# Kernel optimization log

Hardware: AMD Instinct MI355X
Metric: run time of the kernel (lower is better)

The kernel has to match this reference:

```python
import jax, jax.numpy as jnp
import numpy as np

N = 300000   # nodes
D = 128      # in_feats == dim (linears4 consumes attention output)
H = 8        # num_heads
K = 5        # fixed mailbox size (reducer_k pads neighbor list to 5)
EPS = 1e-5


def _layer_norm(x, g, b):
    m = jnp.mean(x, axis=-1, keepdims=True)
    v = jnp.mean((x - m) ** 2, axis=-1, keepdims=True)
    return (x - m) * jax.lax.rsqrt(v + EPS) * g + b


def _self_atten(q, k, v, mask, wq, wk, wv, wo, bo, w1, b1, w2, b2, g1, be1, g2, be2):
    # q: [N,1,D], k/v: [N,K,D], mask: [N,1,1,K] (True = padded key)
    n = q.shape[0]
    dh = D // H
    def heads(x):  # [n, s, D] -> [n, H, s, dh]
        return x.reshape(n, -1, H, dh).transpose(0, 2, 1, 3)
    q1, k1, v1 = heads(q @ wq), heads(k @ wk), heads(v @ wv)
    dots = jnp.einsum('nhqd,nhkd->nhqk', q1, k1) * (dh ** -0.5)
    dots = jnp.where(mask, -jnp.inf, dots)
    attn = jax.nn.softmax(dots, axis=-1)
    out = jnp.einsum('nhqk,nhkd->nhqd', attn, v1)
    out = out.transpose(0, 2, 1, 3).reshape(n, -1, D) @ wo + bo
    x = _layer_norm(q + out, g1, be1)            # residual + norm1
    ffn = jax.nn.relu(x @ w1 + b1) @ w2 + b2
    return _layer_norm(x + ffn, g2, be2)         # residual + norm2


def setup_inputs() -> dict:
    key = jax.random.key(0)
    ks = iter(jax.random.split(key, 64))
    nrm = lambda shape, s=0.05: jax.random.normal(next(ks), shape, jnp.float32) * s
    feat = jax.random.normal(next(ks), (N, D), jnp.float32)
    nbr_idx = jax.random.randint(next(ks), (N, K), 0, N, dtype=jnp.int32)
    deg = jax.random.randint(next(ks), (N,), 1, K + 1)      # in-degree in [1, 5]
    nbr_valid = jnp.arange(K)[None, :] < deg[:, None]        # [N, K] bool
    inp = {'feat': feat, 'nbr_idx': nbr_idx, 'nbr_valid': nbr_valid}
    for i in ('1', '2'):
        inp['wq' + i] = nrm((D, D)); inp['wk' + i] = nrm((D, D)); inp['wv' + i] = nrm((D, D))
        inp['wo' + i] = nrm((D, D)); inp['bo' + i] = jnp.zeros((D,), jnp.float32)
        inp['w' + i + 'a'] = nrm((D, 2 * D)); inp['b' + i + 'a'] = jnp.zeros((2 * D,), jnp.float32)
        inp['w' + i + 'b'] = nrm((2 * D, D)); inp['b' + i + 'b'] = jnp.zeros((D,), jnp.float32)
        inp['g' + i + 'a'] = jnp.ones((D,), jnp.float32); inp['be' + i + 'a'] = jnp.zeros((D,), jnp.float32)
        inp['g' + i + 'b'] = jnp.ones((D,), jnp.float32); inp['be' + i + 'b'] = jnp.zeros((D,), jnp.float32)
    inp['w4'] = nrm((D, D // 2)); inp['b4'] = jnp.zeros((D // 2,), jnp.float32)
    return inp


def reference(feat, nbr_idx, nbr_valid,
              wq1, wk1, wv1, wo1, bo1, w1a, b1a, w1b, b1b, g1a, be1a, g1b, be1b,
              wq2, wk2, wv2, wo2, bo2, w2a, b2a, w2b, b2b, g2a, be2a, g2b, be2b,
              w4, b4):
    # mailbox gather: padded [N, K, D] neighbor features, zeros in padding slots
    k = feat[nbr_idx] * nbr_valid[..., None].astype(feat.dtype)
    q = feat[:, None, :]                                   # [N, 1, D]
    mask = (jnp.sum(k, axis=-1) == 0)[:, None, None, :]    # count_pad -> [N,1,1,K]
    q = _self_atten(q, k, k, mask, wq1, wk1, wv1, wo1, bo1, w1a, b1a, w1b, b1b, g1a, be1a, g1b, be1b)
    out = _self_atten(q, k, k, mask, wq2, wk2, wv2, wo2, bo2, w2a, b2a, w2b, b2b, g2a, be2a, g2b, be2b)
    return jnp.tanh(out[:, 0, :] @ w4 + b4)                # tanh(linears4(hf)) -> [N, D//2]
```

## Files before the change

### kernel.cpp

```cpp
#include <hip/hip_runtime.h>
#include <cstdint>
#include <cmath>

using u16 = unsigned short;
using u8  = unsigned char;
using u32 = unsigned int;

typedef __attribute__((ext_vector_type(8))) short short8;
typedef __attribute__((ext_vector_type(8))) unsigned short u16x8;
typedef __attribute__((ext_vector_type(4))) float f32x4;

#define DEV static __device__ __forceinline__

DEV u16 f2bf(float f) {
  u32 u = __builtin_bit_cast(u32, f);
  u = u + 0x7fffu + ((u >> 16) & 1u);
  return (u16)(u >> 16);
}
DEV float bf2f(u16 h) { return __builtin_bit_cast(float, ((u32)h) << 16); }

template<int NT, int NKB>
DEV void gemm_direct(const u16* __restrict__ wsrc, int ncols,
                     const u16* act, int strideA, int kbase,
                     f32x4* acc, int rt, int cbase, int lane) {
  int l15 = lane & 15, quad = lane >> 4;
  const u16* arow = act + (rt*16 + l15) * strideA + kbase + quad*8;
#pragma unroll
  for (int kb = 0; kb < NKB; ++kb) {
    short8 af = *(const short8*)(arow + kb*32);
    const u16* wrow = wsrc + (size_t)(kb*4 + quad) * ncols * 8;
#pragma unroll
    for (int t = 0; t < NT; ++t) {
      short8 bf = *(const short8*)(wrow + ((cbase + t)*16 + l15) * 8);
      acc[t] = __builtin_amdgcn_mfma_f32_16x16x32_bf16(af, bf, acc[t], 0, 0, 0);
    }
  }
}

DEV void ln_epi(f32x4* acc, float rxf[4][4], int rt, int cbase, int wave, int lane,
                const float* __restrict__ bias, const float* __restrict__ g,
                const float* __restrict__ be, u16* act, float* red) {
  int l15 = lane & 15, quad = lane >> 4;
  int half = wave & 1;
  float v[4][4];
  float s[4] = {0.f,0.f,0.f,0.f}, ss[4] = {0.f,0.f,0.f,0.f};
#pragma unroll
  for (int t = 0; t < 4; ++t) {
    int col = (cbase + t)*16 + l15;
    float b = bias[col];
#pragma unroll
    for (int r = 0; r < 4; ++r) {
      float val = acc[t][r] + b + rxf[t][r];
      v[t][r] = val;
      s[r] += val; ss[r] += val*val;
    }
  }
#pragma unroll
  for (int m = 1; m < 16; m <<= 1) {
#pragma unroll
    for (int r = 0; r < 4; ++r) {
      s[r]  += __shfl_xor(s[r],  m);
      ss[r] += __shfl_xor(ss[r], m);
    }
  }
  if (l15 == 0) {
#pragma unroll
    for (int r = 0; r < 4; ++r) {
      int row = rt*16 + quad*4 + r;
      red[row*4 + half*2 + 0] = s[r];
      red[row*4 + half*2 + 1] = ss[r];
    }
  }
  __syncthreads();
#pragma unroll
  for (int r = 0; r < 4; ++r) {
    int row = rt*16 + quad*4 + r;
    float st  = red[row*4 + 0] + red[row*4 + 2];
    float sst = red[row*4 + 1] + red[row*4 + 3];
    float mean = st * (1.f/128.f);
    float var  = sst * (1.f/128.f) - mean*mean;
    float rs = rsqrtf(var + 1e-5f);
#pragma unroll
    for (int t = 0; t < 4; ++t) {
      int col = (cbase + t)*16 + l15;
      float xn = (v[t][r] - mean) * rs * g[col] + be[col];
      rxf[t][r] = xn;
      act[row*136 + col] = f2bf(xn);
    }
  }
  __syncthreads();
}

DEV void relu_epi(f32x4* acc, int rt, int cbase, int lane,
                  const float* __restrict__ bias, int colbase, u16* h1) {
  int l15 = lane & 15, quad = lane >> 4;
#pragma unroll
  for (int t = 0; t < 4; ++t) {
    int col = (cbase + t)*16 + l15;
    float b = bias[colbase + col];
#pragma unroll
    for (int r = 0; r < 4; ++r) {
      int row = rt*16 + quad*4 + r;
      float val = fmaxf(acc[t][r] + b, 0.f);
      h1[row*264 + colbase + col] = f2bf(val);
    }
  }
}

DEV void q_epi(f32x4* acc, int rt, int cbase, int lane, u16* dst) {
  int l15 = lane & 15, quad = lane >> 4;
#pragma unroll
  for (int t = 0; t < 4; ++t)
#pragma unroll
    for (int r = 0; r < 4; ++r)
      dst[(rt*16 + quad*4 + r)*264 + (cbase + t)*16 + l15] = f2bf(acc[t][r]);
}

DEV void attention(const u16* __restrict__ Pg, const int* s_nidx, const u8* s_nval,
                   const u16* qbuf, u16* act, int layerOff, int tid) {
  int nl = tid >> 3, h = tid & 7;
  float q[16];
  {
    const u16* qp = qbuf + nl*264 + h*16;
    u16x8 q0 = *(const u16x8*)qp;
    u16x8 q1 = *(const u16x8*)(qp + 8);
#pragma unroll
    for (int i = 0; i < 8; ++i) { q[i] = bf2f(q0[i]); q[8+i] = bf2f(q1[i]); }
  }
  float sc[5], w[5];
  int mlist[5], vmask[5];
  float mx = -1e30f;
#pragma unroll
  for (int j = 0; j < 5; ++j) {
    int mj = s_nidx[nl*5 + j];
    int vj = s_nval[nl*5 + j];
    mlist[j] = mj; vmask[j] = vj;
    const u16* kr = Pg + (size_t)mj*512 + layerOff + h*16;
    u16x8 k0 = *(const u16x8*)kr;
    u16x8 k1 = *(const u16x8*)(kr + 8);
    float d = 0.f;
#pragma unroll
    for (int i = 0; i < 8; ++i) d += bf2f(k0[i])*q[i] + bf2f(k1[i])*q[8+i];
    sc[j] = vj ? d * 0.25f : -1e30f;
    mx = fmaxf(mx, sc[j]);
  }
  int anyv = vmask[0] | vmask[1] | vmask[2] | vmask[3] | vmask[4];
  float sum = 0.f;
#pragma unroll
  for (int j = 0; j < 5; ++j) { w[j] = vmask[j] ? __expf(sc[j] - mx) : 0.f; sum += w[j]; }
  float o[16];
#pragma unroll
  for (int i = 0; i < 16; ++i) o[i] = 0.f;
  if (anyv) {
    float inv = 1.f / sum;
#pragma unroll
    for (int j = 0; j < 5; ++j) {
      if (w[j] > 0.f) {
        const u16* vr = Pg + (size_t)mlist[j]*512 + layerOff + 128 + h*16;
        u16x8 v0 = *(const u16x8*)vr;
        u16x8 v1 = *(const u16x8*)(vr + 8);
        float wj = w[j] * inv;
#pragma unroll
        for (int i = 0; i < 8; ++i) { o[i] += wj * bf2f(v0[i]); o[8+i] += wj * bf2f(v1[i]); }
      }
    }
  }
  u16* op = act + nl*136 + h*16;
#pragma unroll
  for (int i = 0; i < 16; ++i) op[i] = f2bf(o[i]);
}

__global__ __launch_bounds__(512) void k1_proj(const float* __restrict__ feat,
                                               u16* __restrict__ P,
                                               const u16* __restrict__ wpack, int N) {
  __shared__ __align__(16) u16 s_act[64*136];
  __shared__ __align__(16) u16 s_c[64*128];
  int tid = threadIdx.x;
  int base = blockIdx.x * 64;
  {
    int row = tid >> 3, c0 = (tid & 7) * 16;
    int n = base + row;
    float v[16];
    if (n < N) {
      const float4* fp = (const float4*)(feat + (size_t)n*128 + c0);
#pragma unroll
      for (int q = 0; q < 4; ++q) { float4 f = fp[q]; v[q*4]=f.x; v[q*4+1]=f.y; v[q*4+2]=f.z; v[q*4+3]=f.w; }
    } else {
#pragma unroll
      for (int i = 0; i < 16; ++i) v[i] = 0.f;
    }
#pragma unroll
    for (int i = 0; i < 16; ++i) s_act[row*136 + c0 + i] = f2bf(v[i]);
  }
  __syncthreads();
  int wave = tid >> 6, lane = tid & 63;
  int rt = wave >> 1, cbase = (wave & 1) * 4;
  int l15 = lane & 15, quad = lane >> 4;
  f32x4 z = {0.f,0.f,0.f,0.f};
  for (int wsel = 0; wsel < 4; ++wsel) {
    f32x4 acc[4] = {z,z,z,z};
    gemm_direct<4,4>(wpack + (size_t)(1 + wsel)*16384, 128, s_act, 136, 0, acc, rt, cbase, lane);
    __syncthreads();
#pragma unroll
    for (int t = 0; t < 4; ++t)
#pragma unroll
      for (int r = 0; r < 4; ++r)
        s_c[(rt*16 + quad*4 + r)*128 + (cbase + t)*16 + l15] = f2bf(acc[t][r]);
    __syncthreads();
    const uint4* src = (const uint4*)s_c;
    for (int i = tid; i < 1024; i += 512) {
      int row = i >> 4, c8 = i & 15;
      int n = base + row;
      if (n < N) *(uint4*)(P + (size_t)n*512 + wsel*128 + c8*8) = src[i];
    }
  }
}

struct K2Args {
  const float* feat; const int* nidx; const void* nval; const int* flag;
  const u16* P; const u16* wpack;
  const float* bo1; const float* b1a; const float* b1b;
  const float* g1a; const float* be1a; const float* g1b; const float* be1b;
  const float* bo2; const float* b2a; const float* b2b;
  const float* g2a; const float* be2a; const float* g2b; const float* be2b;
  const float* b4; float* out; int N;
};

__global__ __launch_bounds__(256) void k2_fused(K2Args a) {
  __shared__ __align__(16) u16   s_act[32*136];
  __shared__ __align__(16) u16   s_h1[32*264];
  __shared__ float s_red[32*4];
  __shared__ int   s_nidx[160];
  __shared__ u8    s_nval[160];

  int tid = threadIdx.x;
  int base = blockIdx.x * 32;
  int wave = tid >> 6, lane = tid & 63;
  int rt = wave >> 1, cb4 = (wave & 1) * 4, cb2 = (wave & 1) * 2;
  int l15 = lane & 15, quad = lane >> 4;

  {
    float* sF = (float*)s_h1;
    int row = tid >> 3, c0 = (tid & 7) * 16;
    int n = base + row;
    float v[16];
    if (n < a.N) {
      const float4* fp = (const float4*)(a.feat + (size_t)n*128 + c0);
#pragma unroll
      for (int q = 0; q < 4; ++q) { float4 f = fp[q]; v[q*4]=f.x; v[q*4+1]=f.y; v[q*4+2]=f.z; v[q*4+3]=f.w; }
    } else {
#pragma unroll
      for (int i = 0; i < 16; ++i) v[i] = 0.f;
    }
#pragma unroll
    for (int i = 0; i < 16; ++i) sF[row*132 + c0 + i] = v[i];
  }
  {
    int mode = *a.flag;
    for (int i = tid; i < 160; i += 256) {
      int n2 = base + i/5;
      int idx = 0; u8 val = 0;
      if (n2 < a.N) {
        size_t e = (size_t)base*5 + i;
        idx = a.nidx[e];
        if (mode == 0)      val = (((const int*)a.nval)[e]   != 0);
        else if (mode == 1) val = (((const float*)a.nval)[e] != 0.f);
        else                val = (((const u8*)a.nval)[e]    != 0);
      }
      s_nidx[i] = idx; s_nval[i] = val;
    }
  }
  __syncthreads();

  float rxf[4][4];
  {
    const float* sF = (const float*)s_h1;
#pragma unroll
    for (int t = 0; t < 4; ++t) {
      int col = (cb4 + t)*16 + l15;
#pragma unroll
      for (int r = 0; r < 4; ++r) {
        int row = rt*16 + quad*4 + r;
        float f = sF[row*132 + col];
        rxf[t][r] = f;
        s_act[row*136 + col] = f2bf(f);
      }
    }
  }
  __syncthreads();

  f32x4 z = {0.f,0.f,0.f,0.f};
  const u16* wp = a.wpack;

  {
    f32x4 acc[4] = {z,z,z,z};
    gemm_direct<4,4>(wp + 0, 128, s_act, 136, 0, acc, rt, cb4, lane);
    q_epi(acc, rt, cb4, lane, s_h1);
    __syncthreads();
  }
  attention(a.P, s_nidx, s_nval, s_h1, s_act, 0, tid);
  __syncthreads();
  {
    f32x4 acc[4] = {z,z,z,z};
    gemm_direct<4,4>(wp + (size_t)5*16384, 128, s_act, 136, 0, acc, rt, cb4, lane);
    ln_epi(acc, rxf, rt, cb4, wave, lane, a.bo1, a.g1a, a.be1a, s_act, s_red);
  }
  {
    f32x4 acc[4] = {z,z,z,z};
    gemm_direct<4,4>(wp + (size_t)6*16384, 128, s_act, 136, 0, acc, rt, cb4, lane);
    relu_epi(acc, rt, cb4, lane, a.b1a, 0, s_h1);
    f32x4 acc2[4] = {z,z,z,z};
    gemm_direct<4,4>(wp + (size_t)7*16384, 128, s_act, 136, 0, acc2, rt, cb4, lane);
    relu_epi(acc2, rt, cb4, lane, a.b1a, 128, s_h1);
    __syncthreads();
  }
  {
    f32x4 acc[4] = {z,z,z,z};
    gemm_direct<4,4>(wp + (size_t)8*16384, 128, s_h1, 264, 0,   acc, rt, cb4, lane);
    gemm_direct<4,4>(wp + (size_t)9*16384, 128, s_h1, 264, 128, acc, rt, cb4, lane);
    ln_epi(acc, rxf, rt, cb4, wave, lane, a.b1b, a.g1b, a.be1b, s_act, s_red);
  }
  {
    f32x4 acc[4] = {z,z,z,z};
    gemm_direct<4,4>(wp + (size_t)10*16384, 128, s_act, 136, 0, acc, rt, cb4, lane);
    q_epi(acc, rt, cb4, lane, s_h1);
    __syncthreads();
  }
  attention(a.P, s_nidx, s_nval, s_h1, s_act, 256, tid);
  __syncthreads();
  {
    f32x4 acc[4] = {z,z,z,z};
    gemm_direct<4,4>(wp + (size_t)11*16384, 128, s_act, 136, 0, acc, rt, cb4, lane);
    ln_epi(acc, rxf, rt, cb4, wave, lane, a.bo2, a.g2a, a.be2a, s_act, s_red);
  }
  {
    f32x4 acc[4] = {z,z,z,z};
    gemm_direct<4,4>(wp + (size_t)12*16384, 128, s_act, 136, 0, acc, rt, cb4, lane);
    relu_epi(acc, rt, cb4, lane, a.b2a, 0, s_h1);
    f32x4 acc2[4] = {z,z,z,z};
    gemm_direct<4,4>(wp + (size_t)13*16384, 128, s_act, 136, 0, acc2, rt, cb4, lane);
    relu_epi(acc2, rt, cb4, lane, a.b2a, 128, s_h1);
    __syncthreads();
  }
  {
    f32x4 acc[4] = {z,z,z,z};
    gemm_direct<4,4>(wp + (size_t)14*16384, 128, s_h1, 264, 0,   acc, rt, cb4, lane);
    gemm_direct<4,4>(wp + (size_t)15*16384, 128, s_h1, 264, 128, acc, rt, cb4, lane);
    ln_epi(acc, rxf, rt, cb4, wave, lane, a.b2b, a.g2b, a.be2b, s_act, s_red);
  }
  {
    f32x4 acc[2] = {z,z};
    gemm_direct<2,4>(wp + (size_t)16*16384, 64, s_act, 136, 0, acc, rt, cb2, lane);
#pragma unroll
    for (int t = 0; t < 2; ++t) {
      int col = (cb2 + t)*16 + l15;
      float b = a.b4[col];
#pragma unroll
      for (int r = 0; r < 4; ++r) {
        int row = rt*16 + quad*4 + r;
        int n = base + row;
        if (n < a.N) a.out[(size_t)n*64 + col] = tanhf(acc[t][r] + b);
      }
    }
  }
}

struct PackDesc { const float* src; int srcStride; int row0; int col0; int ncols; int dstOff; };
struct PackArgs { PackDesc d[17]; };

__global__ void pack_kernel(PackArgs pa, u16* __restrict__ wpack) {
  PackDesc d = pa.d[blockIdx.x];
  int total = 128 * d.ncols;
  for (int e = threadIdx.x; e < total; e += blockDim.x) {
    int k, n;
    if (d.ncols == 128) { k = e >> 7; n = e & 127; }
    else                { k = e >> 6; n = e & 63; }
    float v = d.src[(size_t)(d.row0 + k) * d.srcStride + d.col0 + n];
    int kb = k >> 5, q = (k >> 3) & 3, j = k & 7;
    wpack[d.dstOff + ((kb*4 + q) * d.ncols + n) * 8 + j] = f2bf(v);
  }
}

__global__ void detect_kernel(const u32* __restrict__ nv, int* __restrict__ flag) {
  __shared__ int sInt, sFlt;
  if (threadIdx.x == 0) { sInt = 1; sFlt = 1; }
  __syncthreads();
  int okI = 1, okF = 1;
  for (int i = threadIdx.x; i < 2048; i += blockDim.x) {
    u32 w = nv[i];
    if (w > 1u) okI = 0;
    if (w != 0u && w != 0x3F800000u) okF = 0;
  }
  if (!okI) atomicAnd(&sInt, 0);
  if (!okF) atomicAnd(&sFlt, 0);
  __syncthreads();
  if (threadIdx.x == 0) *flag = sInt ? 0 : (sFlt ? 1 : 2);
}

extern "C" void kernel_launch(void* const* d_in, const int* in_sizes, int n_in,
                              void* d_out, int out_size, void* d_ws, size_t ws_size,
                              hipStream_t stream) {
  const float* feat = (const float*)d_in[0];
  const int*   nidx = (const int*)d_in[1];
  const void*  nval = d_in[2];
  int N = in_sizes[0] / 128;

  u16* P     = (u16*)d_ws;
  u16* wpack = P + (size_t)N * 512;
  int* flag  = (int*)(wpack + (size_t)17 * 16384);

  detect_kernel<<<1, 256, 0, stream>>>((const u32*)nval, flag);

  PackArgs pa;
  int c = 0;
  auto W = [&](int i){ return (const float*)d_in[i]; };
  auto add = [&](const float* src, int stride, int r0, int c0, int ncols){
    pa.d[c] = PackDesc{src, stride, r0, c0, ncols, c * 16384}; ++c;
  };
  add(W(3),  128, 0,   0,   128);
  add(W(4),  128, 0,   0,   128);
  add(W(5),  128, 0,   0,   128);
  add(W(17), 128, 0,   0,   128);
  add(W(18), 128, 0,   0,   128);
  add(W(6),  128, 0,   0,   128);
  add(W(8),  256, 0,   0,   128);
  add(W(8),  256, 0,   128, 128);
  add(W(10), 128, 0,   0,   128);
  add(W(10), 128, 128, 0,   128);
  add(W(16), 128, 0,   0,   128);
  add(W(19), 128, 0,   0,   128);
  add(W(21), 256, 0,   0,   128);
  add(W(21), 256, 0,   128, 128);
  add(W(23), 128, 0,   0,   128);
  add(W(23), 128, 128, 0,   128);
  add(W(29), 64,  0,   0,   64);
  pack_kernel<<<17, 256, 0, stream>>>(pa, wpack);

  k1_proj<<<(N + 63) / 64, 512, 0, stream>>>(feat, P, wpack, N);

  K2Args ka;
  ka.feat = feat; ka.nidx = nidx; ka.nval = nval; ka.flag = flag;
  ka.P = P; ka.wpack = wpack;
  ka.bo1 = W(7);  ka.b1a = W(9);  ka.b1b = W(11);
  ka.g1a = W(12); ka.be1a = W(13); ka.g1b = W(14); ka.be1b = W(15);
  ka.bo2 = W(20); ka.b2a = W(22); ka.b2b = W(24);
  ka.g2a = W(25); ka.be2a = W(26); ka.g2b = W(27); ka.be2b = W(28);
  ka.b4 = W(30); ka.out = (float*)d_out; ka.N = N;
  k2_fused<<<(N + 31) / 32, 256, 0, stream>>>(ka);
}
```

Measured before the change: 1.046 ms.

## Make each wave own 16 full rows to remove block-level barriers

Both kernels are restructured so each wave handles 16 nodes across all 128 output columns, with private shared-memory slices. LayerNorm row reductions then stay inside one wave's shuffles, so the shared reduction buffer and every __syncthreads are removed. Each wave also stages its own features, neighbor lists and attention work, and the residual is read straight from global memory. In exchange each wave holds twice as many accumulators (8 tiles instead of 4), which raises register pressure and may reduce occupancy.

```diff
diff --git a/kernel.cpp b/kernel.cpp
--- a/kernel.cpp
+++ b/kernel.cpp
@@ -8,6 +8,7 @@
 
 typedef __attribute__((ext_vector_type(8))) short short8;
 typedef __attribute__((ext_vector_type(8))) unsigned short u16x8;
+typedef __attribute__((ext_vector_type(4))) unsigned short u16x4;
 typedef __attribute__((ext_vector_type(4))) float f32x4;
 
 #define DEV static __device__ __forceinline__
@@ -20,33 +21,31 @@
 DEV float bf2f(u16 h) { return __builtin_bit_cast(float, ((u32)h) << 16); }
 
 template<int NT, int NKB>
-DEV void gemm_direct(const u16* __restrict__ wsrc, int ncols,
-                     const u16* act, int strideA, int kbase,
-                     f32x4* acc, int rt, int cbase, int lane) {
+DEV void gemm_wave(const u16* __restrict__ wsrc, int ncols,
+                   const u16* actp, int strideA, int kbase,
+                   f32x4* acc, int lane) {
   int l15 = lane & 15, quad = lane >> 4;
-  const u16* arow = act + (rt*16 + l15) * strideA + kbase + quad*8;
+  const u16* arow = actp + l15 * strideA + kbase + quad*8;
 #pragma unroll
   for (int kb = 0; kb < NKB; ++kb) {
     short8 af = *(const short8*)(arow + kb*32);
     const u16* wrow = wsrc + (size_t)(kb*4 + quad) * ncols * 8;
 #pragma unroll
     for (int t = 0; t < NT; ++t) {
-      short8 bf = *(const short8*)(wrow + ((cbase + t)*16 + l15) * 8);
+      short8 bf = *(const short8*)(wrow + (t*16 + l15) * 8);
       acc[t] = __builtin_amdgcn_mfma_f32_16x16x32_bf16(af, bf, acc[t], 0, 0, 0);
     }
   }
 }
 
-DEV void ln_epi(f32x4* acc, float rxf[4][4], int rt, int cbase, int wave, int lane,
-                const float* __restrict__ bias, const float* __restrict__ g,
-                const float* __restrict__ be, u16* act, float* red) {
-  int l15 = lane & 15, quad = lane >> 4;
-  int half = wave & 1;
-  float v[4][4];
+DEV void ln_epi8(f32x4* acc, float rxf[8][4], int l15, int quad,
+                 const float* __restrict__ bias, const float* __restrict__ g,
+                 const float* __restrict__ be, u16* actp) {
+  float v[8][4];
   float s[4] = {0.f,0.f,0.f,0.f}, ss[4] = {0.f,0.f,0.f,0.f};
 #pragma unroll
-  for (int t = 0; t < 4; ++t) {
-    int col = (cbase + t)*16 + l15;
+  for (int t = 0; t < 8; ++t) {
+    int col = t*16 + l15;
     float b = bias[col];
 #pragma unroll
     for (int r = 0; r < 4; ++r) {
@@ -63,154 +62,143 @@
       ss[r] += __shfl_xor(ss[r], m);
     }
   }
-  if (l15 == 0) {
-#pragma unroll
-    for (int r = 0; r < 4; ++r) {
-      int row = rt*16 + quad*4 + r;
-      red[row*4 + half*2 + 0] = s[r];
-      red[row*4 + half*2 + 1] = ss[r];
-    }
-  }
-  __syncthreads();
 #pragma unroll
   for (int r = 0; r < 4; ++r) {
-    int row = rt*16 + quad*4 + r;
-    float st  = red[row*4 + 0] + red[row*4 + 2];
-    float sst = red[row*4 + 1] + red[row*4 + 3];
-    float mean = st * (1.f/128.f);
-    float var  = sst * (1.f/128.f) - mean*mean;
+    int row = quad*4 + r;
+    float mean = s[r] * (1.f/128.f);
+    float var  = ss[r] * (1.f/128.f) - mean*mean;
     float rs = rsqrtf(var + 1e-5f);
 #pragma unroll
-    for (int t = 0; t < 4; ++t) {
-      int col = (cbase + t)*16 + l15;
+    for (int t = 0; t < 8; ++t) {
+      int col = t*16 + l15;
       float xn = (v[t][r] - mean) * rs * g[col] + be[col];
       rxf[t][r] = xn;
-      act[row*136 + col] = f2bf(xn);
-    }
-  }
-  __syncthreads();
-}
-
-DEV void relu_epi(f32x4* acc, int rt, int cbase, int lane,
-                  const float* __restrict__ bias, int colbase, u16* h1) {
-  int l15 = lane & 15, quad = lane >> 4;
-#pragma unroll
-  for (int t = 0; t < 4; ++t) {
-    int col = (cbase + t)*16 + l15;
+      actp[row*136 + col] = f2bf(xn);
+    }
+  }
+}
+
+DEV void relu_epi8(f32x4* acc, int l15, int quad,
+                   const float* __restrict__ bias, int colbase, u16* hb) {
+#pragma unroll
+  for (int t = 0; t < 8; ++t) {
+    int col = t*16 + l15;
     float b = bias[colbase + col];
 #pragma unroll
     for (int r = 0; r < 4; ++r) {
-      int row = rt*16 + quad*4 + r;
-      float val = fmaxf(acc[t][r] + b, 0.f);
-      h1[row*264 + colbase + col] = f2bf(val);
-    }
-  }
-}
-
-DEV void q_epi(f32x4* acc, int rt, int cbase, int lane, u16* dst) {
-  int l15 = lane & 15, quad = lane >> 4;
-#pragma unroll
-  for (int t = 0; t < 4; ++t)
+      int row = quad*4 + r;
+      hb[row*264 + colbase + col] = f2bf(fmaxf(acc[t][r] + b, 0.f));
+    }
+  }
+}
+
+DEV void q_epi8(f32x4* acc, int l15, int quad, u16* hb) {
+#pragma unroll
+  for (int t = 0; t < 8; ++t)
 #pragma unroll
     for (int r = 0; r < 4; ++r)
-      dst[(rt*16 + quad*4 + r)*264 + (cbase + t)*16 + l15] = f2bf(acc[t][r]);
-}
-
-DEV void attention(const u16* __restrict__ Pg, const int* s_nidx, const u8* s_nval,
-                   const u16* qbuf, u16* act, int layerOff, int tid) {
-  int nl = tid >> 3, h = tid & 7;
-  float q[16];
-  {
-    const u16* qp = qbuf + nl*264 + h*16;
-    u16x8 q0 = *(const u16x8*)qp;
-    u16x8 q1 = *(const u16x8*)(qp + 8);
-#pragma unroll
-    for (int i = 0; i < 8; ++i) { q[i] = bf2f(q0[i]); q[8+i] = bf2f(q1[i]); }
-  }
-  float sc[5], w[5];
-  int mlist[5], vmask[5];
-  float mx = -1e30f;
-#pragma unroll
-  for (int j = 0; j < 5; ++j) {
-    int mj = s_nidx[nl*5 + j];
-    int vj = s_nval[nl*5 + j];
-    mlist[j] = mj; vmask[j] = vj;
-    const u16* kr = Pg + (size_t)mj*512 + layerOff + h*16;
-    u16x8 k0 = *(const u16x8*)kr;
-    u16x8 k1 = *(const u16x8*)(kr + 8);
-    float d = 0.f;
-#pragma unroll
-    for (int i = 0; i < 8; ++i) d += bf2f(k0[i])*q[i] + bf2f(k1[i])*q[8+i];
-    sc[j] = vj ? d * 0.25f : -1e30f;
-    mx = fmaxf(mx, sc[j]);
-  }
-  int anyv = vmask[0] | vmask[1] | vmask[2] | vmask[3] | vmask[4];
-  float sum = 0.f;
-#pragma unroll
-  for (int j = 0; j < 5; ++j) { w[j] = vmask[j] ? __expf(sc[j] - mx) : 0.f; sum += w[j]; }
-  float o[16];
-#pragma unroll
-  for (int i = 0; i < 16; ++i) o[i] = 0.f;
-  if (anyv) {
-    float inv = 1.f / sum;
+      hb[(quad*4 + r)*264 + t*16 + l15] = f2bf(acc[t][r]);
+}
+
+DEV void attention_wave(const u16* __restrict__ Pg, const int* nidx, const u8* nval,
+                        const u16* qb, u16* actp, int layerOff, int lane) {
+#pragma unroll
+  for (int p = 0; p < 2; ++p) {
+    int nl = p*8 + (lane >> 3);
+    int hd = lane & 7;
+    float q[16];
+    {
+      const u16* qp = qb + nl*264 + hd*16;
+      u16x8 q0 = *(const u16x8*)qp;
+      u16x8 q1 = *(const u16x8*)(qp + 8);
+#pragma unroll
+      for (int i = 0; i < 8; ++i) { q[i] = bf2f(q0[i]); q[8+i] = bf2f(q1[i]); }
+    }
+    float sc[5], w[5];
+    int mlist[5], vmask[5];
+    float mx = -1e30f;
 #pragma unroll
     for (int j = 0; j < 5; ++j) {
-      if (w[j] > 0.f) {
-        const u16* vr = Pg + (size_t)mlist[j]*512 + layerOff + 128 + h*16;
-        u16x8 v0 = *(const u16x8*)vr;
-        u16x8 v1 = *(const u16x8*)(vr + 8);
-        float wj = w[j] * inv;
-#pragma unroll
-        for (int i = 0; i < 8; ++i) { o[i] += wj * bf2f(v0[i]); o[8+i] += wj * bf2f(v1[i]); }
+      int mj = nidx[nl*5 + j];
+      int vj = nval[nl*5 + j];
+      mlist[j] = mj; vmask[j] = vj;
+      const u16* kr = Pg + (size_t)mj*512 + layerOff + hd*16;
+      u16x8 k0 = *(const u16x8*)kr;
+      u16x8 k1 = *(const u16x8*)(kr + 8);
+      float d = 0.f;
+#pragma unroll
+      for (int i = 0; i < 8; ++i) d += bf2f(k0[i])*q[i] + bf2f(k1[i])*q[8+i];
+      sc[j] = vj ? d * 0.25f : -1e30f;
+      mx = fmaxf(mx, sc[j]);
+    }
+    int anyv = vmask[0] | vmask[1] | vmask[2] | vmask[3] | vmask[4];
+    float sum = 0.f;
+#pragma unroll
+    for (int j = 0; j < 5; ++j) { w[j] = vmask[j] ? __expf(sc[j] - mx) : 0.f; sum += w[j]; }
+    float o[16];
+#pragma unroll
+    for (int i = 0; i < 16; ++i) o[i] = 0.f;
+    if (anyv) {
+      float inv = 1.f / sum;
+#pragma unroll
+      for (int j = 0; j < 5; ++j) {
+        if (w[j] > 0.f) {
+          const u16* vr = Pg + (size_t)mlist[j]*512 + layerOff + 128 + hd*16;
+          u16x8 v0 = *(const u16x8*)vr;
+          u16x8 v1 = *(const u16x8*)(vr + 8);
+          float wj = w[j] * inv;
+#pragma unroll
+          for (int i = 0; i < 8; ++i) { o[i] += wj * bf2f(v0[i]); o[8+i] += wj * bf2f(v1[i]); }
+        }
       }
     }
-  }
-  u16* op = act + nl*136 + h*16;
-#pragma unroll
-  for (int i = 0; i < 16; ++i) op[i] = f2bf(o[i]);
-}
-
-__global__ __launch_bounds__(512) void k1_proj(const float* __restrict__ feat,
+    u16* op = actp + nl*136 + hd*16;
+#pragma unroll
+    for (int i = 0; i < 16; ++i) op[i] = f2bf(o[i]);
+  }
+}
+
+DEV void stage_feat_wave(const float* __restrict__ feat, int nb, int N, u16* actp, int lane) {
+#pragma unroll
+  for (int it = 0; it < 8; ++it) {
+    int i = it*64 + lane;
+    int row = i >> 5, c4 = i & 31;
+    int n = nb + row;
+    float4 f = {0.f,0.f,0.f,0.f};
+    if (n < N) f = *(const float4*)(feat + (size_t)n*128 + c4*4);
+    u16x4 v4 = { f2bf(f.x), f2bf(f.y), f2bf(f.z), f2bf(f.w) };
+    *(u16x4*)(actp + row*136 + c4*4) = v4;
+  }
+}
+
+__global__ __launch_bounds__(256) void k1_proj(const float* __restrict__ feat,
                                                u16* __restrict__ P,
                                                const u16* __restrict__ wpack, int N) {
-  __shared__ __align__(16) u16 s_act[64*136];
-  __shared__ __align__(16) u16 s_c[64*128];
-  int tid = threadIdx.x;
-  int base = blockIdx.x * 64;
-  {
-    int row = tid >> 3, c0 = (tid & 7) * 16;
-    int n = base + row;
-    float v[16];
-    if (n < N) {
-      const float4* fp = (const float4*)(feat + (size_t)n*128 + c0);
-#pragma unroll
-      for (int q = 0; q < 4; ++q) { float4 f = fp[q]; v[q*4]=f.x; v[q*4+1]=f.y; v[q*4+2]=f.z; v[q*4+3]=f.w; }
-    } else {
-#pragma unroll
-      for (int i = 0; i < 16; ++i) v[i] = 0.f;
-    }
-#pragma unroll
-    for (int i = 0; i < 16; ++i) s_act[row*136 + c0 + i] = f2bf(v[i]);
-  }
-  __syncthreads();
-  int wave = tid >> 6, lane = tid & 63;
-  int rt = wave >> 1, cbase = (wave & 1) * 4;
+  __shared__ __align__(16) u16 s_act[4*16*136];
+  __shared__ __align__(16) u16 s_c[4*16*128];
+  int tid = threadIdx.x, wave = tid >> 6, lane = tid & 63;
   int l15 = lane & 15, quad = lane >> 4;
+  u16* actp = s_act + wave*16*136;
+  u16* cbuf = s_c   + wave*16*128;
+  int nb = blockIdx.x*64 + wave*16;
+
+  stage_feat_wave(feat, nb, N, actp, lane);
+
   f32x4 z = {0.f,0.f,0.f,0.f};
   for (int wsel = 0; wsel < 4; ++wsel) {
-    f32x4 acc[4] = {z,z,z,z};
-    gemm_direct<4,4>(wpack + (size_t)(1 + wsel)*16384, 128, s_act, 136, 0, acc, rt, cbase, lane);
-    __syncthreads();
-#pragma unroll
-    for (int t = 0; t < 4; ++t)
+    f32x4 acc[8] = {z,z,z,z,z,z,z,z};
+    gemm_wave<8,4>(wpack + (size_t)(1 + wsel)*16384, 128, actp, 136, 0, acc, lane);
+#pragma unroll
+    for (int t = 0; t < 8; ++t)
 #pragma unroll
       for (int r = 0; r < 4; ++r)
-        s_c[(rt*16 + quad*4 + r)*128 + (cbase + t)*16 + l15] = f2bf(acc[t][r]);
-    __syncthreads();
-    const uint4* src = (const uint4*)s_c;
-    for (int i = tid; i < 1024; i += 512) {
+        cbuf[(quad*4 + r)*128 + t*16 + l15] = f2bf(acc[t][r]);
+    const uint4* src = (const uint4*)cbuf;
+#pragma unroll
+    for (int it = 0; it < 4; ++it) {
+      int i = it*64 + lane;
       int row = i >> 4, c8 = i & 15;
-      int n = base + row;
+      int n = nb + row;
       if (n < N) *(uint4*)(P + (size_t)n*512 + wsel*128 + c8*8) = src[i];
     }
   }
@@ -227,138 +215,111 @@
 };
 
 __global__ __launch_bounds__(256) void k2_fused(K2Args a) {
-  __shared__ __align__(16) u16   s_act[32*136];
-  __shared__ __align__(16) u16   s_h1[32*264];
-  __shared__ float s_red[32*4];
-  __shared__ int   s_nidx[160];
-  __shared__ u8    s_nval[160];
-
-  int tid = threadIdx.x;
-  int base = blockIdx.x * 32;
-  int wave = tid >> 6, lane = tid & 63;
-  int rt = wave >> 1, cb4 = (wave & 1) * 4, cb2 = (wave & 1) * 2;
+  __shared__ __align__(16) u16 s_act[4*16*136];
+  __shared__ __align__(16) u16 s_h[4*16*264];
+  __shared__ int s_nidx[4*80];
+  __shared__ u8  s_nval[4*80];
+
+  int tid = threadIdx.x, wave = tid >> 6, lane = tid & 63;
   int l15 = lane & 15, quad = lane >> 4;
-
-  {
-    float* sF = (float*)s_h1;
-    int row = tid >> 3, c0 = (tid & 7) * 16;
-    int n = base + row;
-    float v[16];
-    if (n < a.N) {
-      const float4* fp = (const float4*)(a.feat + (size_t)n*128 + c0);
-#pragma unroll
-      for (int q = 0; q < 4; ++q) { float4 f = fp[q]; v[q*4]=f.x; v[q*4+1]=f.y; v[q*4+2]=f.z; v[q*4+3]=f.w; }
-    } else {
-#pragma unroll
-      for (int i = 0; i < 16; ++i) v[i] = 0.f;
-    }
-#pragma unroll
-    for (int i = 0; i < 16; ++i) sF[row*132 + c0 + i] = v[i];
-  }
+  u16* actp = s_act + wave*16*136;
+  u16* hb   = s_h   + wave*16*264;
+  int* wn_i = s_nidx + wave*80;
+  u8*  wn_v = s_nval + wave*80;
+  int nb = blockIdx.x*64 + wave*16;
+
+  stage_feat_wave(a.feat, nb, a.N, actp, lane);
+
   {
     int mode = *a.flag;
-    for (int i = tid; i < 160; i += 256) {
-      int n2 = base + i/5;
+    for (int i = lane; i < 80; i += 64) {
+      int n2 = nb + i/5;
       int idx = 0; u8 val = 0;
       if (n2 < a.N) {
-        size_t e = (size_t)base*5 + i;
+        size_t e = (size_t)nb*5 + i;
         idx = a.nidx[e];
         if (mode == 0)      val = (((const int*)a.nval)[e]   != 0);
         else if (mode == 1) val = (((const float*)a.nval)[e] != 0.f);
         else                val = (((const u8*)a.nval)[e]    != 0);
       }
-      s_nidx[i] = idx; s_nval[i] = val;
-    }
-  }
-  __syncthreads();
-
-  float rxf[4][4];
-  {
-    const float* sF = (const float*)s_h1;
-#pragma unroll
-    for (int t = 0; t < 4; ++t) {
-      int col = (cb4 + t)*16 + l15;
-#pragma unroll
-      for (int r = 0; r < 4; ++r) {
-        int row = rt*16 + quad*4 + r;
-        float f = sF[row*132 + col];
-        rxf[t][r] = f;
-        s_act[row*136 + col] = f2bf(f);
-      }
-    }
-  }
-  __syncthreads();
+      wn_i[i] = idx; wn_v[i] = val;
+    }
+  }
+
+  float rxf[8][4];
+#pragma unroll
+  for (int t = 0; t < 8; ++t) {
+    int col = t*16 + l15;
+#pragma unroll
+    for (int r = 0; r < 4; ++r) {
+      int n = nb + quad*4 + r;
+      rxf[t][r] = (n < a.N) ? a.feat[(size_t)n*128 + col] : 0.f;
+    }
+  }
 
   f32x4 z = {0.f,0.f,0.f,0.f};
   const u16* wp = a.wpack;
 
   {
+    f32x4 acc[8] = {z,z,z,z,z,z,z,z};
+    gemm_wave<8,4>(wp + 0, 128, actp, 136, 0, acc, lane);
+    q_epi8(acc, l15, quad, hb);
+  }
+  attention_wave(a.P, wn_i, wn_v, hb, actp, 0, lane);
+  {
+    f32x4 acc[8] = {z,z,z,z,z,z,z,z};
+    gemm_wave<8,4>(wp + (size_t)5*16384, 128, actp, 136, 0, acc, lane);
+    ln_epi8(acc, rxf, l15, quad, a.bo1, a.g1a, a.be1a, actp);
+  }
+  {
+    f32x4 acc[8] = {z,z,z,z,z,z,z,z};
+    gemm_wave<8,4>(wp + (size_t)6*16384, 128, actp, 136, 0, acc, lane);
+    relu_epi8(acc, l15, quad, a.b1a, 0, hb);
+    f32x4 acc2[8] = {z,z,z,z,z,z,z,z};
+    gemm_wave<8,4>(wp + (size_t)7*16384, 128, actp, 136, 0, acc2, lane);
+    relu_epi8(acc2, l15, quad, a.b1a, 128, hb);
+  }
+  {
+    f32x4 acc[8] = {z,z,z,z,z,z,z,z};
+    gemm_wave<8,4>(wp + (size_t)8*16384, 128, hb, 264, 0,   acc, lane);
+    gemm_wave<8,4>(wp + (size_t)9*16384, 128, hb, 264, 128, acc, lane);
+    ln_epi8(acc, rxf, l15, quad, a.b1b, a.g1b, a.be1b, actp);
+  }
+  {
+    f32x4 acc[8] = {z,z,z,z,z,z,z,z};
+    gemm_wave<8,4>(wp + (size_t)10*16384, 128, actp, 136, 0, acc, lane);
+    q_epi8(acc, l15, quad, hb);
+  }
+  attention_wave(a.P, wn_i, wn_v, hb, actp, 256, lane);
+  {
+    f32x4 acc[8] = {z,z,z,z,z,z,z,z};
+    gemm_wave<8,4>(wp + (size_t)11*16384, 128, actp, 136, 0, acc, lane);
+    ln_epi8(acc, rxf, l15, quad, a.bo2, a.g2a, a.be2a, actp);
+  }
+  {
+    f32x4 acc[8] = {z,z,z,z,z,z,z,z};
+    gemm_wave<8,4>(wp + (size_t)12*16384, 128, actp, 136, 0, acc, lane);
+    relu_epi8(acc, l15, quad, a.b2a, 0, hb);
+    f32x4 acc2[8] = {z,z,z,z,z,z,z,z};
+    gemm_wave<8,4>(wp + (size_t)13*16384, 128, actp, 136, 0, acc2, lane);
+    relu_epi8(acc2, l15, quad, a.b2a, 128, hb);
+  }
+  {
+    f32x4 acc[8] = {z,z,z,z,z,z,z,z};
+    gemm_wave<8,4>(wp + (size_t)14*16384, 128, hb, 264, 0,   acc, lane);
+    gemm_wave<8,4>(wp + (size_t)15*16384, 128, hb, 264, 128, acc, lane);
+    ln_epi8(acc, rxf, l15, quad, a.b2b, a.g2b, a.be2b, actp);
+  }
+  {
     f32x4 acc[4] = {z,z,z,z};
-    gemm_direct<4,4>(wp + 0, 128, s_act, 136, 0, acc, rt, cb4, lane);
-    q_epi(acc, rt, cb4, lane, s_h1);
-    __syncthreads();
-  }
-  attention(a.P, s_nidx, s_nval, s_h1, s_act, 0, tid);
-  __syncthreads();
-  {
-    f32x4 acc[4] = {z,z,z,z};
-    gemm_direct<4,4>(wp + (size_t)5*16384, 128, s_act, 136, 0, acc, rt, cb4, lane);
-    ln_epi(acc, rxf, rt, cb4, wave, lane, a.bo1, a.g1a, a.be1a, s_act, s_red);
-  }
-  {
-    f32x4 acc[4] = {z,z,z,z};
-    gemm_direct<4,4>(wp + (size_t)6*16384, 128, s_act, 136, 0, acc, rt, cb4, lane);
-    relu_epi(acc, rt, cb4, lane, a.b1a, 0, s_h1);
-    f32x4 acc2[4] = {z,z,z,z};
-    gemm_direct<4,4>(wp + (size_t)7*16384, 128, s_act, 136, 0, acc2, rt, cb4, lane);
-    relu_epi(acc2, rt, cb4, lane, a.b1a, 128, s_h1);
-    __syncthreads();
-  }
-  {
-    f32x4 acc[4] = {z,z,z,z};
-    gemm_direct<4,4>(wp + (size_t)8*16384, 128, s_h1, 264, 0,   acc, rt, cb4, lane);
-    gemm_direct<4,4>(wp + (size_t)9*16384, 128, s_h1, 264, 128, acc, rt, cb4, lane);
-    ln_epi(acc, rxf, rt, cb4, wave, lane, a.b1b, a.g1b, a.be1b, s_act, s_red);
-  }
-  {
-    f32x4 acc[4] = {z,z,z,z};
-    gemm_direct<4,4>(wp + (size_t)10*16384, 128, s_act, 136, 0, acc, rt, cb4, lane);
-    q_epi(acc, rt, cb4, lane, s_h1);
-    __syncthreads();
-  }
-  attention(a.P, s_nidx, s_nval, s_h1, s_act, 256, tid);
-  __syncthreads();
-  {
-    f32x4 acc[4] = {z,z,z,z};
-    gemm_direct<4,4>(wp + (size_t)11*16384, 128, s_act, 136, 0, acc, rt, cb4, lane);
-    ln_epi(acc, rxf, rt, cb4, wave, lane, a.bo2, a.g2a, a.be2a, s_act, s_red);
-  }
-  {
-    f32x4 acc[4] = {z,z,z,z};
-    gemm_direct<4,4>(wp + (size_t)12*16384, 128, s_act, 136, 0, acc, rt, cb4, lane);
-    relu_epi(acc, rt, cb4, lane, a.b2a, 0, s_h1);
-    f32x4 acc2[4] = {z,z,z,z};
-    gemm_direct<4,4>(wp + (size_t)13*16384, 128, s_act, 136, 0, acc2, rt, cb4, lane);
-    relu_epi(acc2, rt, cb4, lane, a.b2a, 128, s_h1);
-    __syncthreads();
-  }
-  {
-    f32x4 acc[4] = {z,z,z,z};
-    gemm_direct<4,4>(wp + (size_t)14*16384, 128, s_h1, 264, 0,   acc, rt, cb4, lane);
-    gemm_direct<4,4>(wp + (size_t)15*16384, 128, s_h1, 264, 128, acc, rt, cb4, lane);
-    ln_epi(acc, rxf, rt, cb4, wave, lane, a.b2b, a.g2b, a.be2b, s_act, s_red);
-  }
-  {
-    f32x4 acc[2] = {z,z};
-    gemm_direct<2,4>(wp + (size_t)16*16384, 64, s_act, 136, 0, acc, rt, cb2, lane);
-#pragma unroll
-    for (int t = 0; t < 2; ++t) {
-      int col = (cb2 + t)*16 + l15;
+    gemm_wave<4,4>(wp + (size_t)16*16384, 64, actp, 136, 0, acc, lane);
+#pragma unroll
+    for (int t = 0; t < 4; ++t) {
+      int col = t*16 + l15;
       float b = a.b4[col];
 #pragma unroll
       for (int r = 0; r < 4; ++r) {
-        int row = rt*16 + quad*4 + r;
-        int n = base + row;
+        int n = nb + quad*4 + r;
         if (n < a.N) a.out[(size_t)n*64 + col] = tanhf(acc[t][r] + b);
       }
     }
@@ -436,7 +397,7 @@
   add(W(29), 64,  0,   0,   64);
   pack_kernel<<<17, 256, 0, stream>>>(pa, wpack);
 
-  k1_proj<<<(N + 63) / 64, 512, 0, stream>>>(feat, P, wpack, N);
+  k1_proj<<<(N + 63) / 64, 256, 0, stream>>>(feat, P, wpack, N);
 
   K2Args ka;
   ka.feat = feat; ka.nidx = nidx; ka.nval = nval; ka.flag = flag;
@@ -446,5 +407,5 @@
   ka.bo2 = W(20); ka.b2a = W(22); ka.b2b = W(24);
   ka.g2a = W(25); ka.be2a = W(26); ka.g2b = W(27); ka.be2b = W(28);
   ka.b4 = W(30); ka.out = (float*)d_out; ka.N = N;
-  k2_fused<<<(N + 31) / 32, 256, 0, stream>>>(ka);
-}
+  k2_fused<<<(N + 63) / 64, 256, 0, stream>>>(ka);
+}
```

Result: slower. 1.416 ms (+35.4%).
